# Kernel optimization log

Hardware: AMD Instinct MI355X
Metric: run time of the kernel (lower is better)

## Reference

```python
import jax, jax.numpy as jnp
import numpy as np

B, S, D, H = 4, 2048, 1024, 16
DK = D // H


def setup_inputs() -> dict:
    key = jax.random.key(0)
    ks = jax.random.split(key, 11)
    s = 1.0 / np.sqrt(D)
    return {
        "x_Q": jax.random.normal(ks[0], (B, S, D), jnp.float32),
        "x_K": jax.random.normal(ks[1], (B, S, D), jnp.float32),
        "x_V": jax.random.normal(ks[2], (B, S, D), jnp.float32),
        "Wq": jax.random.normal(ks[3], (D, D), jnp.float32) * s,
        "bq": jax.random.normal(ks[4], (D,), jnp.float32) * 0.01,
        "Wk": jax.random.normal(ks[5], (D, D), jnp.float32) * s,
        "bk": jax.random.normal(ks[6], (D,), jnp.float32) * 0.01,
        "Wv": jax.random.normal(ks[7], (D, D), jnp.float32) * s,
        "bv": jax.random.normal(ks[8], (D,), jnp.float32) * 0.01,
        "Wo": jax.random.normal(ks[9], (D, D), jnp.float32) * s,
        "bo": jax.random.normal(ks[10], (D,), jnp.float32) * 0.01,
    }


def reference(x_Q, x_K, x_V, Wq, bq, Wk, bk, Wv, bv, Wo, bo):
    def heads(x, W, b):
        # [B,S,D] -> [B,H,S,DK]
        y = x @ W.T + b
        return y.reshape(B, S, H, DK).transpose(0, 2, 1, 3)

    Q = heads(x_Q, Wq, bq)
    K = heads(x_K, Wk, bk)
    V = heads(x_V, Wv, bv)
    scores = jnp.einsum('bhqd,bhkd->bhqk', Q, K) / jnp.sqrt(jnp.float32(DK))
    probs = jax.nn.softmax(scores, axis=-1)
    out = jnp.einsum('bhqk,bhkd->bhqd', probs, V)
    out = out.transpose(0, 2, 1, 3).reshape(B, S, D)
    return out @ Wo.T + bo
```

## Files before the change

### kernel.cpp

```cpp
#include <hip/hip_runtime.h>

typedef __attribute__((ext_vector_type(8))) short bf16x8;
typedef __attribute__((ext_vector_type(4))) short short4v;
typedef __attribute__((ext_vector_type(4))) float f32x4;
typedef __attribute__((ext_vector_type(16))) float f32x16;
typedef __attribute__((ext_vector_type(2))) unsigned int u32x2;

#define DEV static __device__ __forceinline__

#define QSC 0.1804165017087941f

DEV unsigned short f2b(float f) {
  union { float f; unsigned int i; } v; v.f = f;
  unsigned int x = v.i;
  return (unsigned short)((x + 0x7FFFu + ((x >> 16) & 1u)) >> 16);
}

DEV void cp16(const unsigned short* g, unsigned short* l) {
  __builtin_amdgcn_global_load_lds(
      (const __attribute__((address_space(1))) void*)g,
      (__attribute__((address_space(3))) void*)l, 16, 0, 0);
}

DEV unsigned int cvtpk(float lo, float hi) {
  unsigned int r;
  asm("v_cvt_pk_bf16_f32 %0, %1, %2" : "=v"(r) : "v"(lo), "v"(hi));
  return r;
}

__global__ void cvt_kernel(const float* __restrict__ in,
                           unsigned short* __restrict__ out, int n, float scale) {
  const int i = (blockIdx.x * blockDim.x + threadIdx.x) * 4;
  if (i < n) {
    const float4 v = *(const float4*)&in[i];
    short4v o;
    o[0] = (short)f2b(v.x * scale); o[1] = (short)f2b(v.y * scale);
    o[2] = (short)f2b(v.z * scale); o[3] = (short)f2b(v.w * scale);
    *(short4v*)&out[i] = o;
  }
}

__global__ void cvt_all(const float* __restrict__ xq, const float* __restrict__ xk,
                        const float* __restrict__ xv, const float* __restrict__ wq,
                        const float* __restrict__ wk, const float* __restrict__ wv,
                        const float* __restrict__ wo, unsigned short* __restrict__ X,
                        unsigned short* __restrict__ W) {
  const int b = blockIdx.x;
  const float* p;
  unsigned short* out;
  float scale = 1.f;
  int i;
  if (b < 24576) {
    const int seg = b >> 13, ib = b & 8191;
    p = (seg == 0) ? xq : (seg == 1) ? xk : xv;
    out = X + (size_t)seg * 8388608;
    i = (ib * 256 + threadIdx.x) * 4;
  } else {
    const int bb = b - 24576;
    const int seg = bb >> 10, ib = bb & 1023;
    p = (seg == 0) ? wq : (seg == 1) ? wk : (seg == 2) ? wv : wo;
    out = W + (size_t)seg * 1048576;
    if (seg == 0) scale = QSC;
    i = (ib * 256 + threadIdx.x) * 4;
  }
  const float4 v = *(const float4*)&p[i];
  short4v o;
  o[0] = (short)f2b(v.x * scale); o[1] = (short)f2b(v.y * scale);
  o[2] = (short)f2b(v.z * scale); o[3] = (short)f2b(v.w * scale);
  *(short4v*)&out[i] = o;
}

#define G256_STAGE(KT, DA, DB)                                                 \
  _Pragma("unroll") for (int is = 0; is < 4; ++is) {                           \
    const int r = is * 64 + srow;                                              \
    cp16(&A[(size_t)(bm + r) * K + (KT) + ssrc], &DA[r * 64 + sdst]);          \
    cp16(&W[(size_t)(bn + r) * K + (KT) + ssrc], &DB[r * 64 + sdst]);          \
  }

template <int MODE>
DEV void gemm256_body(const unsigned short* __restrict__ A,
                      const unsigned short* __restrict__ W,
                      const float* __restrict__ bias, void* __restrict__ OutV,
                      unsigned short* sA0, unsigned short* sA1,
                      unsigned short* sB0, unsigned short* sB1,
                      int bm, int bn, int N, int K, float bsc) {
  const int tid = threadIdx.x;
  const int lane = tid & 63, wid = tid >> 6;
  const int lr = lane & 15, quad = lane >> 4;
  const int wm = (wid >> 2) * 128;
  const int wn = (wid & 3) * 64;
  const int srow = tid >> 3;
  const int sdst = (tid & 7) * 8;
  const int ssrc = ((tid & 7) ^ (srow & 7)) * 8;

  f32x4 acc[8][4] = {};

  unsigned short *cA = sA0, *cB = sB0, *nA = sA1, *nB = sB1;
  const int nk = K >> 6;

  G256_STAGE(0, cA, cB);

  for (int t = 0; t < nk; ++t) {
    if (t + 1 < nk) {
      G256_STAGE((t + 1) << 6, nA, nB);
      asm volatile("s_waitcnt vmcnt(8)" ::: "memory");
    } else {
      asm volatile("s_waitcnt vmcnt(0)" ::: "memory");
    }
    __builtin_amdgcn_s_barrier();
    __builtin_amdgcn_sched_barrier(0);

#pragma unroll
    for (int ks = 0; ks < 2; ++ks) {
      bf16x8 af[8], bf[4];
      const int co = (((ks * 4 + quad) ^ (lr & 7)) << 3);
#pragma unroll
      for (int i = 0; i < 8; ++i)
        af[i] = *(const bf16x8*)&cA[(wm + i * 16 + lr) * 64 + co];
#pragma unroll
      for (int j = 0; j < 4; ++j)
        bf[j] = *(const bf16x8*)&cB[(wn + j * 16 + lr) * 64 + co];
      __builtin_amdgcn_s_setprio(1);
#pragma unroll
      for (int i = 0; i < 8; ++i)
#pragma unroll
        for (int j = 0; j < 4; ++j)
          acc[i][j] = __builtin_amdgcn_mfma_f32_16x16x32_bf16(af[i], bf[j], acc[i][j], 0, 0, 0);
      __builtin_amdgcn_s_setprio(0);
    }

    __builtin_amdgcn_s_barrier();
    __builtin_amdgcn_sched_barrier(0);
    unsigned short* tA = cA; cA = nA; nA = tA;
    unsigned short* tB = cB; cB = nB; nB = tB;
  }

#pragma unroll
  for (int j = 0; j < 4; ++j) {
    const int n = bn + wn + j * 16 + lr;
    const float bv = bias[n] * bsc;
#pragma unroll
    for (int i = 0; i < 8; ++i) {
      const int mb = bm + wm + i * 16 + quad * 4;
      if (MODE == 2) {
        u32x2 w;
        w[0] = cvtpk(acc[i][j][0] + bv, acc[i][j][1] + bv);
        w[1] = cvtpk(acc[i][j][2] + bv, acc[i][j][3] + bv);
        *(u32x2*)&((unsigned short*)OutV)[
            ((size_t)((mb >> 11) * 16 + (n >> 6)) * 64 + (n & 63)) * 2048 + (mb & 2047)] = w;
      } else {
#pragma unroll
        for (int r = 0; r < 4; ++r) {
          const int m = mb + r;
          const float o = acc[i][j][r] + bv;
          if (MODE == 0) {
            ((float*)OutV)[(size_t)m * N + n] = o;
          } else {
            ((unsigned short*)OutV)[((size_t)((m >> 11) * 16 + (n >> 6)) * 2048 + (m & 2047)) * 64 + (n & 63)] = f2b(o);
          }
        }
      }
    }
  }
}

__global__ __launch_bounds__(512, 2) void gemm256_out(
    const unsigned short* __restrict__ A, const unsigned short* __restrict__ W,
    const float* __restrict__ bias, void* __restrict__ OutV, int N, int K) {
  __shared__ __align__(16) unsigned short sA[2][256 * 64];
  __shared__ __align__(16) unsigned short sB[2][256 * 64];
  const int wg = blockIdx.x + (blockIdx.y << 5);
  const int xcd = wg & 7;
  const int j = wg >> 3;
  const int bn = (j & 3) * 256;
  const int bm = (xcd * 4 + (j >> 2)) * 256;
  gemm256_body<0>(A, W, bias, OutV, &sA[0][0], &sA[1][0], &sB[0][0], &sB[1][0],
                  bm, bn, N, K, 1.f);
}

__global__ __launch_bounds__(512, 2) void gemm256_qkv(
    const unsigned short* __restrict__ Aall, const unsigned short* __restrict__ Wall,
    const float* __restrict__ b0, const float* __restrict__ b1,
    const float* __restrict__ b2, unsigned short* __restrict__ Out) {
  __shared__ __align__(16) unsigned short sA[2][256 * 64];
  __shared__ __align__(16) unsigned short sB[2][256 * 64];
  const int wg = blockIdx.x + (blockIdx.y << 5) + (blockIdx.z << 7);
  const int xcd = wg & 7;
  const int j = wg >> 3;
  const int bn = (j & 3) * 256;
  const int g = xcd * 12 + (j >> 2);
  const int z = g >> 5;
  const int bm = (g & 31) * 256;
  const unsigned short* A = Aall + (size_t)z * 8388608;
  const unsigned short* W = Wall + (size_t)z * 1048576;
  const float* bias = (z == 0) ? b0 : (z == 1) ? b1 : b2;
  const float bsc = (z == 0) ? QSC : 1.f;
  void* OutV = (void*)(Out + (size_t)z * 8388608);
  if (z == 2)
    gemm256_body<2>(A, W, bias, OutV, &sA[0][0], &sA[1][0], &sB[0][0], &sB[1][0],
                    bm, bn, 1024, 1024, bsc);
  else
    gemm256_body<1>(A, W, bias, OutV, &sA[0][0], &sA[1][0], &sB[0][0], &sB[1][0],
                    bm, bn, 1024, 1024, bsc);
}

template <int MODE>
DEV void gemm_tile_body(const unsigned short* __restrict__ A,
                        const unsigned short* __restrict__ W,
                        const float* __restrict__ bias, void* __restrict__ OutV,
                        unsigned short* sA, unsigned short* sB,
                        int bm, int bn, int N, int K, float bsc) {
  const int tid = threadIdx.x;
  const int lane = tid & 63, wave = tid >> 6;
  const int lr = lane & 15, quad = lane >> 4;
  const int wm = (wave >> 1) * 64, wn = (wave & 1) * 64;
  const int srow = tid >> 3;
  const int sdst = (tid & 7) * 8;
  const int ssrc = ((tid & 7) ^ (srow & 7)) * 8;

  f32x4 acc[4][4] = {};

  for (int kt = 0; kt < K; kt += 64) {
#pragma unroll
    for (int is = 0; is < 4; ++is) {
      const int r = is * 32 + srow;
      cp16(&A[(size_t)(bm + r) * K + kt + ssrc], &sA[r * 64 + sdst]);
      cp16(&W[(size_t)(bn + r) * K + kt + ssrc], &sB[r * 64 + sdst]);
    }
    __syncthreads();
#pragma unroll
    for (int ks = 0; ks < 2; ++ks) {
      bf16x8 af[4], bf[4];
      const int co = (((ks * 4 + quad) ^ (lr & 7)) << 3);
#pragma unroll
      for (int i = 0; i < 4; ++i)
        af[i] = *(const bf16x8*)&sA[(wm + i * 16 + lr) * 64 + co];
#pragma unroll
      for (int j = 0; j < 4; ++j)
        bf[j] = *(const bf16x8*)&sB[(wn + j * 16 + lr) * 64 + co];
#pragma unroll
      for (int i = 0; i < 4; ++i)
#pragma unroll
        for (int j = 0; j < 4; ++j)
          acc[i][j] = __builtin_amdgcn_mfma_f32_16x16x32_bf16(af[i], bf[j], acc[i][j], 0, 0, 0);
    }
    __syncthreads();
  }

#pragma unroll
  for (int j = 0; j < 4; ++j) {
    const int n = bn + wn + j * 16 + lr;
    const float bv = bias[n] * bsc;
#pragma unroll
    for (int i = 0; i < 4; ++i) {
      const int mb = bm + wm + i * 16 + quad * 4;
      if (MODE == 2) {
        u32x2 w;
        w[0] = cvtpk(acc[i][j][0] + bv, acc[i][j][1] + bv);
        w[1] = cvtpk(acc[i][j][2] + bv, acc[i][j][3] + bv);
        *(u32x2*)&((unsigned short*)OutV)[
            ((size_t)((mb >> 11) * 16 + (n >> 6)) * 64 + (n & 63)) * 2048 + (mb & 2047)] = w;
      } else {
#pragma unroll
        for (int r = 0; r < 4; ++r) {
          const int m = mb + r;
          const float o = acc[i][j][r] + bv;
          if (MODE == 0) {
            ((float*)OutV)[(size_t)m * N + n] = o;
          } else {
            ((unsigned short*)OutV)[((size_t)((m >> 11) * 16 + (n >> 6)) * 2048 + (m & 2047)) * 64 + (n & 63)] = f2b(o);
          }
        }
      }
    }
  }
}

template <int MODE>
__global__ __launch_bounds__(256, 3) void gemm_bt(
    const unsigned short* __restrict__ A, const unsigned short* __restrict__ W,
    const float* __restrict__ bias, void* __restrict__ OutV,
    int N, int K, float bsc) {
  __shared__ __align__(16) unsigned short sA[128 * 64];
  __shared__ __align__(16) unsigned short sB[128 * 64];
  const int wg = blockIdx.x + (blockIdx.y << 6);
  const int xcd = wg & 7;
  const int j = wg >> 3;
  const int bn = (j & 7) * 128;
  const int bm = (xcd * 8 + (j >> 3)) * 128;
  gemm_tile_body<MODE>(A, W, bias, OutV, sA, sB, bm, bn, N, K, bsc);
}

#define ATTN_PACK8(SREG, RB, KD)                                               \
  {                                                                            \
    float pr[8];                                                               \
    _Pragma("unroll") for (int r = 0; r < 8; ++r) {                            \
      pr[r] = __builtin_amdgcn_exp2f(SREG[(RB) + r]);                          \
      rsp[r & 3] += pr[r];                                                     \
    }                                                                          \
    const u32x2 w02 = __builtin_amdgcn_permlane32_swap(                        \
        cvtpk(pr[0], pr[1]), cvtpk(pr[4], pr[5]), false, false);               \
    const u32x2 w13 = __builtin_amdgcn_permlane32_swap(                        \
        cvtpk(pr[2], pr[3]), cvtpk(pr[6], pr[7]), false, false);               \
    pa[KD].w[0] = w02[0]; pa[KD].w[1] = w13[0];                                \
    pa[KD].w[2] = w02[1]; pa[KD].w[3] = w13[1];                                \
  }

#define ATTN_TILE(T, SKB, SVB, DKB, DVB)                                       \
  {                                                                            \
    if ((T) + 1 < 32) {                                                        \
      const int kvn = ((T) + 1) * 64;                                          \
      _Pragma("unroll") for (int is = 0; is < 2; ++is) {                       \
        const int r = is * 32 + sr_;                                           \
        const int sw = (sc_ ^ ((r ^ (r >> 3)) & 7)) * 8;                       \
        cp16(&Kp[(size_t)(kvn + r) * 64 + sw], &DKB[r * 64 + sc_ * 8]);        \
        cp16(&Vp[(size_t)r * 2048 + kvn + sw], &DVB[r * 64 + sc_ * 8]);        \
      }                                                                        \
    }                                                                          \
    {                                                                          \
      f32x16 s0 = {};                                                          \
      __builtin_amdgcn_s_setprio(1);                                           \
      _Pragma("unroll") for (int ks = 0; ks < 4; ++ks) {                       \
        const bf16x8 k0 = *(const bf16x8*)&SKB[rowa + (((ks * 2 + b5) ^ swa) << 3)]; \
        s0 = __builtin_amdgcn_mfma_f32_32x32x16_bf16(k0, qf[ks], s0, 0, 0, 0); \
      }                                                                        \
      __builtin_amdgcn_s_setprio(0);                                           \
      ATTN_PACK8(s0, 0, 0)                                                     \
      ATTN_PACK8(s0, 8, 1)                                                     \
    }                                                                          \
    __builtin_amdgcn_s_setprio(1);                                             \
    _Pragma("unroll") for (int ks = 0; ks < 2; ++ks) {                         \
      const bf16x8 va = *(const bf16x8*)&SVB[rowa + (((ks * 2 + b5) ^ swa) << 3)]; \
      const bf16x8 vb = *(const bf16x8*)&SVB[rowb + (((ks * 2 + b5) ^ swb) << 3)]; \
      oacc0 = __builtin_amdgcn_mfma_f32_32x32x16_bf16(pa[ks].v, va, oacc0, 0, 0, 0); \
      oacc1 = __builtin_amdgcn_mfma_f32_32x32x16_bf16(pa[ks].v, vb, oacc1, 0, 0, 0); \
    }                                                                          \
    __builtin_amdgcn_s_setprio(0);                                             \
    {                                                                          \
      f32x16 s1 = {};                                                          \
      __builtin_amdgcn_s_setprio(1);                                           \
      _Pragma("unroll") for (int ks = 0; ks < 4; ++ks) {                       \
        const bf16x8 k1 = *(const bf16x8*)&SKB[rowb + (((ks * 2 + b5) ^ swb) << 3)]; \
        s1 = __builtin_amdgcn_mfma_f32_32x32x16_bf16(k1, qf[ks], s1, 0, 0, 0); \
      }                                                                        \
      __builtin_amdgcn_s_setprio(0);                                           \
      ATTN_PACK8(s1, 0, 0)                                                     \
      ATTN_PACK8(s1, 8, 1)                                                     \
    }                                                                          \
    __builtin_amdgcn_s_setprio(1);                                             \
    _Pragma("unroll") for (int ks = 2; ks < 4; ++ks) {                         \
      const bf16x8 va = *(const bf16x8*)&SVB[rowa + (((ks * 2 + b5) ^ swa) << 3)]; \
      const bf16x8 vb = *(const bf16x8*)&SVB[rowb + (((ks * 2 + b5) ^ swb) << 3)]; \
      oacc0 = __builtin_amdgcn_mfma_f32_32x32x16_bf16(pa[ks - 2].v, va, oacc0, 0, 0, 0); \
      oacc1 = __builtin_amdgcn_mfma_f32_32x32x16_bf16(pa[ks - 2].v, vb, oacc1, 0, 0, 0); \
    }                                                                          \
    __builtin_amdgcn_s_setprio(0);                                             \
    __syncthreads();                                                           \
  }

__global__ __launch_bounds__(256, 3) void attn_kernel(
    const unsigned short* __restrict__ Qb, const unsigned short* __restrict__ Kb,
    const unsigned short* __restrict__ Vt, unsigned short* __restrict__ Ob) {
  __shared__ __align__(16) unsigned short sK[2][64 * 64];
  __shared__ __align__(16) unsigned short sV[2][64 * 64];

  const int tid = threadIdx.x;
  const int lane = tid & 63;
  const int wave = tid >> 6;
  const int c31 = lane & 31;
  const int b5 = lane >> 5;

  const int wg = blockIdx.y * 16 + blockIdx.x;
  const int j = wg >> 3;
  const int bh = (wg & 7) * 8 + (j >> 4);
  const int q0 = (j & 15) * 128 + wave * 32;

  const size_t base = (size_t)bh * (2048 * 64);
  const unsigned short* __restrict__ Qp = Qb + base;
  const unsigned short* __restrict__ Kp = Kb + base;
  const unsigned short* __restrict__ Vp = Vt + base;

  bf16x8 qf[4];
#pragma unroll
  for (int ks = 0; ks < 4; ++ks)
    qf[ks] = *(const bf16x8*)&Qp[(size_t)(q0 + c31) * 64 + ks * 16 + b5 * 8];

  f32x16 oacc0 = {}, oacc1 = {};
  float rsp[4] = {0.f, 0.f, 0.f, 0.f};
  union PA { unsigned int w[4]; bf16x8 v; };
  PA pa[2];

  const int sr_ = tid >> 3;
  const int sc_ = tid & 7;

  const int swa = (c31 ^ (c31 >> 3)) & 7;
  const int swb = swa ^ 4;
  const int rowa = c31 * 64, rowb = (32 + c31) * 64;

  unsigned short* sK0 = &sK[0][0];
  unsigned short* sK1 = &sK[1][0];
  unsigned short* sV0 = &sV[0][0];
  unsigned short* sV1 = &sV[1][0];

#pragma unroll
  for (int is = 0; is < 2; ++is) {
    const int r = is * 32 + sr_;
    const int sw = (sc_ ^ ((r ^ (r >> 3)) & 7)) * 8;
    cp16(&Kp[(size_t)r * 64 + sw], &sK0[r * 64 + sc_ * 8]);
    cp16(&Vp[(size_t)r * 2048 + sw], &sV0[r * 64 + sc_ * 8]);
  }
  __syncthreads();

  for (int t = 0; t < 32; t += 2) {
    ATTN_TILE(t, sK0, sV0, sK1, sV1);
    ATTN_TILE(t + 1, sK1, sV1, sK0, sV0);
  }

  float rs = (rsp[0] + rsp[1]) + (rsp[2] + rsp[3]);
  rs += __shfl_xor(rs, 32);
  const float linv = 1.f / rs;
  const int b = bh >> 4, h = bh & 15;
#pragma unroll
  for (int r = 0; r < 16; ++r) {
    const int crow = (r & 3) + 8 * (r >> 2) + 4 * b5;
    const float li = __shfl(linv, crow);
    unsigned short* op = &Ob[(size_t)(b * 2048 + q0 + crow) * 1024 + h * 64];
    op[c31] = f2b(oacc0[r] * li);
    op[32 + c31] = f2b(oacc1[r] * li);
  }
}

extern "C" void kernel_launch(void* const* d_in, const int* in_sizes, int n_in,
                              void* d_out, int out_size, void* d_ws, size_t ws_size,
                              hipStream_t stream) {
  const float* xq = (const float*)d_in[0];
  const float* xk = (const float*)d_in[1];
  const float* xv = (const float*)d_in[2];
  const float* Wq = (const float*)d_in[3];
  const float* bq = (const float*)d_in[4];
  const float* Wk = (const float*)d_in[5];
  const float* bk = (const float*)d_in[6];
  const float* Wv = (const float*)d_in[7];
  const float* bv = (const float*)d_in[8];
  const float* Wo = (const float*)d_in[9];
  const float* bo = (const float*)d_in[10];

  unsigned short* ws = (unsigned short*)d_ws;
  const size_t SZ = (size_t)8192 * 1024;
  const size_t WSZ = (size_t)1024 * 1024;

  if (ws_size >= (6 * SZ + 4 * WSZ) * sizeof(unsigned short)) {
    unsigned short* Xall = ws;
    unsigned short* Wall = ws + 3 * SZ;
    unsigned short* Qb = Wall + 4 * WSZ;
    unsigned short* Kb = Qb + SZ;
    unsigned short* Vt = Kb + SZ;

    hipLaunchKernelGGL(cvt_all, dim3(28672), dim3(256), 0, stream,
                       xq, xk, xv, Wq, Wk, Wv, Wo, Xall, Wall);
    hipLaunchKernelGGL(gemm256_qkv, dim3(32, 4, 3), dim3(512), 0, stream,
                       Xall, Wall, bq, bk, bv, Qb);
    hipLaunchKernelGGL(attn_kernel, dim3(16, 64), dim3(256), 0, stream, Qb, Kb, Vt, Xall);
    hipLaunchKernelGGL(gemm256_out, dim3(32, 4), dim3(512), 0, stream,
                       Xall, Wall + 3 * WSZ, bo, d_out, 1024, 1024);
  } else {
    unsigned short* X  = ws;
    unsigned short* Wb = ws + SZ;
    unsigned short* Qb = ws + SZ + SZ / 8;
    unsigned short* Kb = Qb + SZ;
    unsigned short* Vt = Kb + SZ;

    const int NX = 8192 * 1024, NW = 1024 * 1024;
    dim3 cbx(256), cgx(NX / 1024), cgw(NW / 1024);
    dim3 gg(64, 8), bb(256);

    hipLaunchKernelGGL(cvt_kernel, cgx, cbx, 0, stream, xq, X, NX, 1.f);
    hipLaunchKernelGGL(cvt_kernel, cgw, cbx, 0, stream, Wq, Wb, NW, QSC);
    hipLaunchKernelGGL((gemm_bt<1>), gg, bb, 0, stream, X, Wb, bq, (void*)Qb, 1024, 1024, QSC);

    hipLaunchKernelGGL(cvt_kernel, cgx, cbx, 0, stream, xk, X, NX, 1.f);
    hipLaunchKernelGGL(cvt_kernel, cgw, cbx, 0, stream, Wk, Wb, NW, 1.f);
    hipLaunchKernelGGL((gemm_bt<1>), gg, bb, 0, stream, X, Wb, bk, (void*)Kb, 1024, 1024, 1.f);

    hipLaunchKernelGGL(cvt_kernel, cgx, cbx, 0, stream, xv, X, NX, 1.f);
    hipLaunchKernelGGL(cvt_kernel, cgw, cbx, 0, stream, Wv, Wb, NW, 1.f);
    hipLaunchKernelGGL((gemm_bt<2>), gg, bb, 0, stream, X, Wb, bv, (void*)Vt, 1024, 1024, 1.f);

    hipLaunchKernelGGL(attn_kernel, dim3(16, 64), bb, 0, stream, Qb, Kb, Vt, X);

    hipLaunchKernelGGL(cvt_kernel, cgw, cbx, 0, stream, Wo, Wb, NW, 1.f);
    hipLaunchKernelGGL((gemm_bt<0>), gg, bb, 0, stream, X, Wb, bo, d_out, 1024, 1024, 1.f);
  }
}
```

Baseline: 348.6 us.

## Split 256-tile GEMM K-step into quarter phases with staggered A prefetch

```diff
diff --git a/kernel.cpp b/kernel.cpp
--- a/kernel.cpp
+++ b/kernel.cpp
@@ -70,19 +70,24 @@
   *(short4v*)&out[i] = o;
 }
 
-#define G256_STAGE(KT, DA, DB)                                                 \
-  _Pragma("unroll") for (int is = 0; is < 4; ++is) {                           \
-    const int r = is * 64 + srow;                                              \
-    cp16(&A[(size_t)(bm + r) * K + (KT) + ssrc], &DA[r * 64 + sdst]);          \
-    cp16(&W[(size_t)(bn + r) * K + (KT) + ssrc], &DB[r * 64 + sdst]);          \
+#define G256_TSZ (256 * 64)
+
+#define STAGE_HALF_A(DST, KT, H)                                               \
+  _Pragma("unroll") for (int is_ = 0; is_ < 2; ++is_) {                        \
+    const int r_ = (H) * 128 + is_ * 64 + srow;                                \
+    cp16(&A[(size_t)(bm + r_) * K + (KT) + ssrc], &DST[r_ * 64 + sdst]);       \
+  }
+#define STAGE_HALF_B(DST, KT, H)                                               \
+  _Pragma("unroll") for (int is_ = 0; is_ < 2; ++is_) {                        \
+    const int r_ = (H) * 128 + is_ * 64 + srow;                                \
+    cp16(&W[(size_t)(bn + r_) * K + (KT) + ssrc], &DST[r_ * 64 + sdst]);       \
   }
 
 template <int MODE>
 DEV void gemm256_body(const unsigned short* __restrict__ A,
                       const unsigned short* __restrict__ W,
                       const float* __restrict__ bias, void* __restrict__ OutV,
-                      unsigned short* sA0, unsigned short* sA1,
-                      unsigned short* sB0, unsigned short* sB1,
+                      unsigned short* sA, unsigned short* sB,
                       int bm, int bn, int N, int K, float bsc) {
   const int tid = threadIdx.x;
   const int lane = tid & 63, wid = tid >> 6;
@@ -94,45 +99,79 @@
   const int ssrc = ((tid & 7) ^ (srow & 7)) * 8;
 
   f32x4 acc[8][4] = {};
-
-  unsigned short *cA = sA0, *cB = sB0, *nA = sA1, *nB = sB1;
   const int nk = K >> 6;
 
-  G256_STAGE(0, cA, cB);
+  STAGE_HALF_B((&sB[0]), 0, 0) STAGE_HALF_B((&sB[0]), 0, 1)
+  STAGE_HALF_A((&sA[0]), 0, 0) STAGE_HALF_A((&sA[0]), 0, 1)
 
   for (int t = 0; t < nk; ++t) {
-    if (t + 1 < nk) {
-      G256_STAGE((t + 1) << 6, nA, nB);
-      asm volatile("s_waitcnt vmcnt(8)" ::: "memory");
+    const unsigned short* ca = &sA[(t & 1) * G256_TSZ];
+    const unsigned short* cb = &sB[(t & 1) * G256_TSZ];
+    unsigned short* na = &sA[((t + 1) & 1) * G256_TSZ];
+    unsigned short* nb = &sB[((t + 1) & 1) * G256_TSZ];
+    const int ktn = (t + 1) << 6;
+    const bool pf = (t + 1 < nk);
+
+    if (pf) {
+      STAGE_HALF_B(nb, ktn, 0) STAGE_HALF_B(nb, ktn, 1)
+      asm volatile("s_waitcnt vmcnt(4)" ::: "memory");
     } else {
       asm volatile("s_waitcnt vmcnt(0)" ::: "memory");
     }
     __builtin_amdgcn_s_barrier();
     __builtin_amdgcn_sched_barrier(0);
 
+    bf16x8 bf[2][4], af[2][2];
 #pragma unroll
     for (int ks = 0; ks < 2; ++ks) {
-      bf16x8 af[8], bf[4];
       const int co = (((ks * 4 + quad) ^ (lr & 7)) << 3);
 #pragma unroll
-      for (int i = 0; i < 8; ++i)
-        af[i] = *(const bf16x8*)&cA[(wm + i * 16 + lr) * 64 + co];
-#pragma unroll
       for (int j = 0; j < 4; ++j)
-        bf[j] = *(const bf16x8*)&cB[(wn + j * 16 + lr) * 64 + co];
-      __builtin_amdgcn_s_setprio(1);
-#pragma unroll
-      for (int i = 0; i < 8; ++i)
-#pragma unroll
-        for (int j = 0; j < 4; ++j)
-          acc[i][j] = __builtin_amdgcn_mfma_f32_16x16x32_bf16(af[i], bf[j], acc[i][j], 0, 0, 0);
-      __builtin_amdgcn_s_setprio(0);
-    }
-
+        bf[ks][j] = *(const bf16x8*)&cb[(wn + j * 16 + lr) * 64 + co];
+#pragma unroll
+      for (int ii = 0; ii < 2; ++ii)
+        af[ks][ii] = *(const bf16x8*)&ca[(wm + ii * 16 + lr) * 64 + co];
+    }
+    asm volatile("s_waitcnt lgkmcnt(0)" ::: "memory");
+    __builtin_amdgcn_sched_barrier(0);
+    __builtin_amdgcn_s_setprio(1);
+#pragma unroll
+    for (int ii = 0; ii < 2; ++ii)
+#pragma unroll
+      for (int j = 0; j < 4; ++j) {
+        acc[ii][j] = __builtin_amdgcn_mfma_f32_16x16x32_bf16(af[0][ii], bf[0][j], acc[ii][j], 0, 0, 0);
+        acc[ii][j] = __builtin_amdgcn_mfma_f32_16x16x32_bf16(af[1][ii], bf[1][j], acc[ii][j], 0, 0, 0);
+      }
+    __builtin_amdgcn_s_setprio(0);
     __builtin_amdgcn_s_barrier();
     __builtin_amdgcn_sched_barrier(0);
-    unsigned short* tA = cA; cA = nA; nA = tA;
-    unsigned short* tB = cB; cB = nB; nB = tB;
+
+#pragma unroll
+    for (int q = 1; q < 4; ++q) {
+#pragma unroll
+      for (int ks = 0; ks < 2; ++ks) {
+        const int co = (((ks * 4 + quad) ^ (lr & 7)) << 3);
+#pragma unroll
+        for (int ii = 0; ii < 2; ++ii)
+          af[ks][ii] = *(const bf16x8*)&ca[(wm + (q * 2 + ii) * 16 + lr) * 64 + co];
+      }
+      if (pf && q == 1) { STAGE_HALF_A(na, ktn, 0) }
+      if (pf && q == 2) { STAGE_HALF_A(na, ktn, 1) }
+      __builtin_amdgcn_s_barrier();
+      asm volatile("s_waitcnt lgkmcnt(0)" ::: "memory");
+      __builtin_amdgcn_sched_barrier(0);
+      __builtin_amdgcn_s_setprio(1);
+#pragma unroll
+      for (int ii = 0; ii < 2; ++ii)
+#pragma unroll
+        for (int j = 0; j < 4; ++j) {
+          acc[q * 2 + ii][j] = __builtin_amdgcn_mfma_f32_16x16x32_bf16(af[0][ii], bf[0][j], acc[q * 2 + ii][j], 0, 0, 0);
+          acc[q * 2 + ii][j] = __builtin_amdgcn_mfma_f32_16x16x32_bf16(af[1][ii], bf[1][j], acc[q * 2 + ii][j], 0, 0, 0);
+        }
+      __builtin_amdgcn_s_setprio(0);
+      __builtin_amdgcn_s_barrier();
+      __builtin_amdgcn_sched_barrier(0);
+    }
   }
 
 #pragma unroll
@@ -164,7 +203,7 @@
   }
 }
 
-__global__ __launch_bounds__(512, 2) void gemm256_out(
+__global__ __launch_bounds__(512, 1) void gemm256_out(
     const unsigned short* __restrict__ A, const unsigned short* __restrict__ W,
     const float* __restrict__ bias, void* __restrict__ OutV, int N, int K) {
   __shared__ __align__(16) unsigned short sA[2][256 * 64];
@@ -174,11 +213,10 @@
   const int j = wg >> 3;
   const int bn = (j & 3) * 256;
   const int bm = (xcd * 4 + (j >> 2)) * 256;
-  gemm256_body<0>(A, W, bias, OutV, &sA[0][0], &sA[1][0], &sB[0][0], &sB[1][0],
-                  bm, bn, N, K, 1.f);
-}
-
-__global__ __launch_bounds__(512, 2) void gemm256_qkv(
+  gemm256_body<0>(A, W, bias, OutV, &sA[0][0], &sB[0][0], bm, bn, N, K, 1.f);
+}
+
+__global__ __launch_bounds__(512, 1) void gemm256_qkv(
     const unsigned short* __restrict__ Aall, const unsigned short* __restrict__ Wall,
     const float* __restrict__ b0, const float* __restrict__ b1,
     const float* __restrict__ b2, unsigned short* __restrict__ Out) {
@@ -197,11 +235,9 @@
   const float bsc = (z == 0) ? QSC : 1.f;
   void* OutV = (void*)(Out + (size_t)z * 8388608);
   if (z == 2)
-    gemm256_body<2>(A, W, bias, OutV, &sA[0][0], &sA[1][0], &sB[0][0], &sB[1][0],
-                    bm, bn, 1024, 1024, bsc);
+    gemm256_body<2>(A, W, bias, OutV, &sA[0][0], &sB[0][0], bm, bn, 1024, 1024, bsc);
   else
-    gemm256_body<1>(A, W, bias, OutV, &sA[0][0], &sA[1][0], &sB[0][0], &sB[1][0],
-                    bm, bn, 1024, 1024, bsc);
+    gemm256_body<1>(A, W, bias, OutV, &sA[0][0], &sB[0][0], bm, bn, 1024, 1024, bsc);
 }
 
 template <int MODE>
```

New measurement: 361.4 us. 3.7% more time.
